# Kernel optimization log

Hardware: AMD Instinct MI355X
Metric: run time of the kernel (lower is better)

Reference implementation:

```python
import jax, jax.numpy as jnp
import numpy as np

DIM = 1024
NUM_HEADS = 16
HEAD_DIM = DIM // NUM_HEADS
SCALE = HEAD_DIM ** -0.5


def setup_inputs() -> dict:
    key = jax.random.key(0)
    ks = jax.random.split(key, 9)
    s = 1.0 / np.sqrt(DIM)
    x = jax.random.normal(ks[0], (2, 2048, DIM), dtype=jnp.float32)
    Wq = jax.random.normal(ks[1], (DIM, DIM), dtype=jnp.float32) * s
    Wk = jax.random.normal(ks[2], (DIM, DIM), dtype=jnp.float32) * s
    Wv = jax.random.normal(ks[3], (DIM, DIM), dtype=jnp.float32) * s
    Wp = jax.random.normal(ks[4], (DIM, DIM), dtype=jnp.float32) * s
    bq = jax.random.normal(ks[5], (DIM,), dtype=jnp.float32) * s
    bk = jax.random.normal(ks[6], (DIM,), dtype=jnp.float32) * s
    bv = jax.random.normal(ks[7], (DIM,), dtype=jnp.float32) * s
    bp = jax.random.normal(ks[8], (DIM,), dtype=jnp.float32) * s
    return {"x": x, "Wq": Wq, "bq": bq, "Wk": Wk, "bk": bk,
            "Wv": Wv, "bv": bv, "Wp": Wp, "bp": bp}


def reference(x, Wq, bq, Wk, bk, Wv, bv, Wp, bp):
    B, L, C = x.shape
    H, D = NUM_HEADS, HEAD_DIM
    # Linear projections (torch Linear: x @ W.T + b)
    q = x @ Wq.T + bq
    k = x @ Wk.T + bk
    v = x @ Wv.T + bv
    # (B, L, H*D) -> (B, H, L, D)
    q = q.reshape(B, L, H, D).transpose(0, 2, 1, 3)
    k = k.reshape(B, L, H, D).transpose(0, 2, 1, 3)
    v = v.reshape(B, L, H, D).transpose(0, 2, 1, 3)
    # scaled dot-product attention, full L x L scores (as in source)
    attn = jnp.einsum('bhqd,bhkd->bhqk', q, k) * SCALE
    attn = jax.nn.softmax(attn, axis=-1)
    out = jnp.einsum('bhqk,bhkd->bhqd', attn, v)
    out = out.transpose(0, 2, 1, 3).reshape(B, L, C)
    return out @ Wp.T + bp
```

## Files before the change

kernel.cpp:

```cpp
#include <hip/hip_runtime.h>

#define DIMC 1024
#define SEQL 2048
#define NB   2
#define NH   16
#define HD   64
#define MTOT (NB*SEQL)
#define XSTR 2048
static constexpr float SM_SCALE = 0.125f;
static constexpr float LOG2E    = 1.4426950408889634f;
static constexpr float QSCALE   = SM_SCALE * LOG2E;

typedef short s16x8 __attribute__((ext_vector_type(8)));
typedef short s16x4 __attribute__((ext_vector_type(4)));
typedef float f32x4 __attribute__((ext_vector_type(4)));
typedef int   i32x4 __attribute__((ext_vector_type(4)));

__device__ __forceinline__ unsigned short f2bf(float f) {
    unsigned int u = __float_as_uint(f);
    u += 0x7fffu + ((u >> 16) & 1u);
    return (unsigned short)(u >> 16);
}
__device__ __forceinline__ s16x8 ld8(const unsigned short* p) {
    return *(const s16x8*)p;
}
__device__ __forceinline__ void gld_lds16(const unsigned short* g, unsigned short* l) {
    __builtin_amdgcn_global_load_lds(
        (const __attribute__((address_space(1))) void*)g,
        (__attribute__((address_space(3))) void*)l, 16, 0, 0);
}

__global__ __launch_bounds__(256) void cast_all(
    const float* __restrict__ x,
    const float* __restrict__ Wq, const float* __restrict__ Wk,
    const float* __restrict__ Wv, const float* __restrict__ Wp,
    const float* __restrict__ bq, const float* __restrict__ bk,
    const float* __restrict__ bvv,
    unsigned short* __restrict__ xb, unsigned short* __restrict__ wall,
    float* __restrict__ ball)
{
    const int bid = blockIdx.x, tid = threadIdx.x;
    if (bid < 4096) {
        int i = bid * 256 + tid;
        float4 f = ((const float4*)x)[i];
        s16x4 o;
        o[0] = (short)f2bf(f.x); o[1] = (short)f2bf(f.y);
        o[2] = (short)f2bf(f.z); o[3] = (short)f2bf(f.w);
        ((s16x4*)xb)[i] = o;
    } else if (bid < 8192) {
        int j = (bid - 4096) * 256 + tid;
        int r = j >> 18;
        const float* src = (r == 0) ? Wq : (r == 1) ? Wk : (r == 2) ? Wv : Wp;
        float4 f = ((const float4*)src)[j & 262143];
        s16x4 o;
        o[0] = (short)f2bf(f.x); o[1] = (short)f2bf(f.y);
        o[2] = (short)f2bf(f.z); o[3] = (short)f2bf(f.w);
        ((s16x4*)wall)[j] = o;
    } else {
        int t2 = (bid - 8192) * 256 + tid;
        if (t2 < 3072)
            ball[t2] = (t2 < 1024) ? bq[t2]
                     : (t2 < 2048) ? bk[t2 - 1024] : bvv[t2 - 2048];
    }
}

__global__ __launch_bounds__(256) void gemm_tile(
    const unsigned short* __restrict__ A, int astride,
    const unsigned short* __restrict__ Wb,
    const float* __restrict__ bias,
    unsigned short* qk, unsigned short* vtb, float* outf, int mode)
{
    __shared__ __align__(16) unsigned short Asm[128 * 32];
    __shared__ __align__(16) unsigned short Bsm[128 * 32];

    const int t    = threadIdx.x;
    const int lane = t & 63;
    const int l15  = lane & 15;
    const int quad = lane >> 4;
    const int w    = t >> 6;
    const int mrow = (w & 1) * 64;
    const int ncol = (w >> 1) * 64;
    const int mt   = blockIdx.x & 31;
    const int nt   = blockIdx.x >> 5;
    const int row0 = mt * 128;

    const unsigned short* ga = A  + (size_t)(row0 + (t >> 2)) * astride + (t & 3) * 8;
    const unsigned short* gb = Wb + (size_t)(nt * 128 + (t >> 2)) * DIMC + (t & 3) * 8;
    const size_t gaStep = (size_t)64 * astride;
    const size_t gbStep = (size_t)64 * DIMC;

    f32x4 acc[4][4] = {};

    for (int k0 = 0; k0 < DIMC; k0 += 32) {
        gld_lds16(ga + k0,          Asm + t * 8);
        gld_lds16(ga + gaStep + k0, Asm + 2048 + t * 8);
        gld_lds16(gb + k0,          Bsm + t * 8);
        gld_lds16(gb + gbStep + k0, Bsm + 2048 + t * 8);
        __syncthreads();

        s16x8 a[4], b[4];
#pragma unroll
        for (int mi = 0; mi < 4; ++mi)
            a[mi] = *(const s16x8*)(Asm + (mrow + mi * 16 + l15) * 32 + quad * 8);
#pragma unroll
        for (int ni = 0; ni < 4; ++ni)
            b[ni] = *(const s16x8*)(Bsm + (ncol + ni * 16 + l15) * 32 + quad * 8);
#pragma unroll
        for (int mi = 0; mi < 4; ++mi)
#pragma unroll
            for (int ni = 0; ni < 4; ++ni)
                acc[mi][ni] = __builtin_amdgcn_mfma_f32_16x16x32_bf16(
                    a[mi], b[ni], acc[mi][ni], 0, 0, 0);
        __syncthreads();
    }

    const int proj = nt >> 3;
#pragma unroll
    for (int ni = 0; ni < 4; ++ni) {
        const int cq = (nt & 7) * 128 + ncol + ni * 16 + l15;
        const float bz = bias[proj * 1024 + cq];
#pragma unroll
        for (int mi = 0; mi < 4; ++mi) {
            const int rbase = row0 + mrow + mi * 16 + quad * 4;
            if (mode == 0) {
                if (proj < 2) {
                    const float scale = (proj == 0) ? QSCALE : 1.0f;
#pragma unroll
                    for (int r = 0; r < 4; ++r)
                        qk[(size_t)(rbase + r) * XSTR + proj * DIMC + cq] =
                            f2bf((acc[mi][ni][r] + bz) * scale);
                } else {
                    const int h = cq >> 6, d = cq & 63;
                    const int bb = rbase >> 11, ll = rbase & (SEQL - 1);
                    s16x4 v4;
                    v4[0] = (short)f2bf(acc[mi][ni][0] + bz);
                    v4[1] = (short)f2bf(acc[mi][ni][1] + bz);
                    v4[2] = (short)f2bf(acc[mi][ni][2] + bz);
                    v4[3] = (short)f2bf(acc[mi][ni][3] + bz);
                    *(s16x4*)(vtb + ((size_t)((bb * NH + h) * HD + d)) * SEQL + ll) = v4;
                }
            } else {
#pragma unroll
                for (int r = 0; r < 4; ++r)
                    outf[(size_t)(rbase + r) * DIMC + cq] = acc[mi][ni][r] + bz;
            }
        }
    }
}

__global__ __launch_bounds__(128) void attn_fused(
    unsigned short* xqk,
    const unsigned short* __restrict__ vt)
{
    __shared__ __align__(16) unsigned short Ksm[2][64 * 64];
    __shared__ __align__(16) unsigned short Vsm[2][64 * 64];

    const int t    = threadIdx.x;
    const int lane = t & 63;
    const int l15  = lane & 15;
    const int quad = lane >> 4;
    const int w    = t >> 6;

    const int bh = blockIdx.x >> 5;
    const int qb = blockIdx.x & 31;
    const int h  = bh & (NH - 1);
    const int bb = bh >> 4;
    const int q0A = qb * 64 + w * 16;
    const int q0B = q0A + 32;

    unsigned short* qbase = xqk + (size_t)(bb * SEQL) * XSTR + h * HD + quad * 8;
    unsigned short* qrA = qbase + (size_t)(q0A + l15) * XSTR;
    unsigned short* qrB = qbase + (size_t)(q0B + l15) * XSTR;
    const s16x8 bqA0 = ld8(qrA), bqA1 = ld8(qrA + 32);
    const s16x8 bqB0 = ld8(qrB), bqB1 = ld8(qrB + 32);

    const int tr = t >> 3, tp = t & 7;
    const int swz = (tp ^ (tr & 7)) * 8;
    const unsigned short* kg = xqk + (size_t)bb * SEQL * XSTR + DIMC + h * HD
                               + (size_t)tr * XSTR + swz;
    const unsigned short* vg = vt + (size_t)(bh * HD + tr) * SEQL + swz;

    f32x4 oA[4] = {}, oB[4] = {};
    float lsA = 0.f, lsB = 0.f;
    const int xk = l15 & 7;

#pragma unroll
    for (int g = 0; g < 4; ++g) {
        gld_lds16(kg + (size_t)(g * 16) * XSTR, Ksm[0] + g * 1024 + t * 8);
        gld_lds16(vg + (size_t)(g * 16) * SEQL, Vsm[0] + g * 1024 + t * 8);
    }
    __syncthreads();

    for (int j0 = 0; j0 < SEQL; j0 += 64) {
        const int cur = (j0 >> 6) & 1, nxt = cur ^ 1;
        if (j0 + 64 < SEQL) {
            const int jn = j0 + 64;
#pragma unroll
            for (int g = 0; g < 4; ++g) {
                gld_lds16(kg + (size_t)(jn + g * 16) * XSTR, Ksm[nxt] + g * 1024 + t * 8);
                gld_lds16(vg + (size_t)(g * 16) * SEQL + jn,  Vsm[nxt] + g * 1024 + t * 8);
            }
        }
        const unsigned short* Kc = Ksm[cur];
        const unsigned short* Vc = Vsm[cur];

#pragma unroll
        for (int hf = 0; hf < 2; ++hf) {
            const int k0 = (hf * 32 + l15) * 64;
            const int k1 = (hf * 32 + 16 + l15) * 64;
            s16x8 a00 = *(const s16x8*)(Kc + k0 + ((quad       ^ xk) * 8));
            s16x8 a01 = *(const s16x8*)(Kc + k0 + (((quad + 4) ^ xk) * 8));
            s16x8 a10 = *(const s16x8*)(Kc + k1 + ((quad       ^ xk) * 8));
            s16x8 a11 = *(const s16x8*)(Kc + k1 + (((quad + 4) ^ xk) * 8));

            s16x8 bv[4];
#pragma unroll
            for (int c = 0; c < 4; ++c) {
                const unsigned short* va = Vc + (c * 16 + l15) * 64 + (quad & 1) * 4;
                const int kc0 = hf * 4 + (quad >> 1);
                s16x4 v0 = *(const s16x4*)(va + ((kc0       ^ xk) * 8));
                s16x4 v1 = *(const s16x4*)(va + (((kc0 + 2) ^ xk) * 8));
                bv[c] = __builtin_shufflevector(v0, v1, 0, 1, 2, 3, 4, 5, 6, 7);
            }

            {
                f32x4 st0 = {}, st1 = {};
                st0 = __builtin_amdgcn_mfma_f32_16x16x32_bf16(a00, bqA0, st0, 0, 0, 0);
                st0 = __builtin_amdgcn_mfma_f32_16x16x32_bf16(a01, bqA1, st0, 0, 0, 0);
                st1 = __builtin_amdgcn_mfma_f32_16x16x32_bf16(a10, bqA0, st1, 0, 0, 0);
                st1 = __builtin_amdgcn_mfma_f32_16x16x32_bf16(a11, bqA1, st1, 0, 0, 0);
                unsigned int t0[4], t1[4];
#pragma unroll
                for (int r = 0; r < 4; ++r) {
                    t0[r] = __float_as_uint(__builtin_amdgcn_exp2f(st0[r])) & 0xffff0000u;
                    t1[r] = __float_as_uint(__builtin_amdgcn_exp2f(st1[r])) & 0xffff0000u;
                    lsA += __uint_as_float(t0[r]) + __uint_as_float(t1[r]);
                }
                i32x4 api;
                api[0] = (int)((t0[0] >> 16) | t0[1]);
                api[1] = (int)((t0[2] >> 16) | t0[3]);
                api[2] = (int)((t1[0] >> 16) | t1[1]);
                api[3] = (int)((t1[2] >> 16) | t1[3]);
                s16x8 ap = __builtin_bit_cast(s16x8, api);
#pragma unroll
                for (int c = 0; c < 4; ++c)
                    oA[c] = __builtin_amdgcn_mfma_f32_16x16x32_bf16(ap, bv[c], oA[c], 0, 0, 0);
            }
            {
                f32x4 st0 = {}, st1 = {};
                st0 = __builtin_amdgcn_mfma_f32_16x16x32_bf16(a00, bqB0, st0, 0, 0, 0);
                st0 = __builtin_amdgcn_mfma_f32_16x16x32_bf16(a01, bqB1, st0, 0, 0, 0);
                st1 = __builtin_amdgcn_mfma_f32_16x16x32_bf16(a10, bqB0, st1, 0, 0, 0);
                st1 = __builtin_amdgcn_mfma_f32_16x16x32_bf16(a11, bqB1, st1, 0, 0, 0);
                unsigned int t0[4], t1[4];
#pragma unroll
                for (int r = 0; r < 4; ++r) {
                    t0[r] = __float_as_uint(__builtin_amdgcn_exp2f(st0[r])) & 0xffff0000u;
                    t1[r] = __float_as_uint(__builtin_amdgcn_exp2f(st1[r])) & 0xffff0000u;
                    lsB += __uint_as_float(t0[r]) + __uint_as_float(t1[r]);
                }
                i32x4 api;
                api[0] = (int)((t0[0] >> 16) | t0[1]);
                api[1] = (int)((t0[2] >> 16) | t0[3]);
                api[2] = (int)((t1[0] >> 16) | t1[1]);
                api[3] = (int)((t1[2] >> 16) | t1[3]);
                s16x8 ap = __builtin_bit_cast(s16x8, api);
#pragma unroll
                for (int c = 0; c < 4; ++c)
                    oB[c] = __builtin_amdgcn_mfma_f32_16x16x32_bf16(ap, bv[c], oB[c], 0, 0, 0);
            }
        }
        __syncthreads();
    }

    lsA += __shfl_xor(lsA, 16);  lsA += __shfl_xor(lsA, 32);
    lsB += __shfl_xor(lsB, 16);  lsB += __shfl_xor(lsB, 32);

    float liA[4], liB[4];
#pragma unroll
    for (int r = 0; r < 4; ++r) {
        liA[r] = 1.0f / __shfl(lsA, quad * 4 + r, 64);
        liB[r] = 1.0f / __shfl(lsB, quad * 4 + r, 64);
    }

#pragma unroll
    for (int c = 0; c < 4; ++c) {
        const int d = c * 16 + l15;
#pragma unroll
        for (int r = 0; r < 4; ++r) {
            const int qr = quad * 4 + r;
            xqk[(size_t)(bb * SEQL + q0A + qr) * XSTR + h * HD + d] = f2bf(oA[c][r] * liA[r]);
            xqk[(size_t)(bb * SEQL + q0B + qr) * XSTR + h * HD + d] = f2bf(oB[c][r] * liB[r]);
        }
    }
}

extern "C" void kernel_launch(void* const* d_in, const int* in_sizes, int n_in,
                              void* d_out, int out_size, void* d_ws, size_t ws_size,
                              hipStream_t stream) {
    const float* x  = (const float*)d_in[0];
    const float* Wq = (const float*)d_in[1];
    const float* bq = (const float*)d_in[2];
    const float* Wk = (const float*)d_in[3];
    const float* bk = (const float*)d_in[4];
    const float* Wv = (const float*)d_in[5];
    const float* bv = (const float*)d_in[6];
    const float* Wp = (const float*)d_in[7];
    const float* bp = (const float*)d_in[8];
    float* out = (float*)d_out;
    unsigned short* vtb = (unsigned short*)d_out;
    unsigned short* xqk = (unsigned short*)d_in[0];

    unsigned short* ws   = (unsigned short*)d_ws;
    const size_t XELT = (size_t)MTOT * DIMC;
    const size_t WELT = (size_t)DIMC * DIMC;
    unsigned short* xb   = ws;
    unsigned short* wall = ws + XELT;
    float*          ball = (float*)(ws + 2 * XELT);

    cast_all<<<8204, 256, 0, stream>>>(x, Wq, Wk, Wv, Wp, bq, bk, bv, xb, wall, ball);

    gemm_tile<<<768, 256, 0, stream>>>(xb, DIMC, wall, ball, xqk, vtb, nullptr, 0);

    attn_fused<<<NB * NH * (SEQL / 64), 128, 0, stream>>>(xqk, vtb);

    gemm_tile<<<256, 256, 0, stream>>>(xqk, XSTR, wall + 3 * WELT, bp,
                                       nullptr, nullptr, out, 1);
}
```

Before: 229.4 us.

## Compute softmax row sums via MFMA with ones, packed bf16 convert, XCD-aware block mapping

The softmax denominator is now accumulated by an extra MFMA against a vector of bf16 ones instead of scalar VALU adds, which also removes the final cross-lane shuffles. The exp results are packed with v_cvt_pk_bf16_f32 (round-to-nearest) instead of truncation masks and shifts. Blocks are remapped so consecutive block IDs on the same XCD share a batch-head, aiming at better L2 reuse of K/V. The change trades VALU work for one extra MFMA per tile and slightly alters rounding.

```diff
diff --git a/kernel.cpp b/kernel.cpp
--- a/kernel.cpp
+++ b/kernel.cpp
@@ -28,6 +28,11 @@
     __builtin_amdgcn_global_load_lds(
         (const __attribute__((address_space(1))) void*)g,
         (__attribute__((address_space(3))) void*)l, 16, 0, 0);
+}
+__device__ __forceinline__ unsigned int cvtpk(float lo, float hi) {
+    unsigned int r;
+    asm("v_cvt_pk_bf16_f32 %0, %1, %2" : "=v"(r) : "v"(lo), "v"(hi));
+    return r;
 }
 
 __global__ __launch_bounds__(256) void cast_all(
@@ -161,8 +166,10 @@
     const int quad = lane >> 4;
     const int w    = t >> 6;
 
-    const int bh = blockIdx.x >> 5;
-    const int qb = blockIdx.x & 31;
+    const int xcd = blockIdx.x & 7;
+    const int ii  = blockIdx.x >> 3;
+    const int bh  = (xcd << 2) | (ii >> 5);
+    const int qb  = ii & 31;
     const int h  = bh & (NH - 1);
     const int bb = bh >> 4;
     const int q0A = qb * 64 + w * 16;
@@ -174,6 +181,10 @@
     const s16x8 bqA0 = ld8(qrA), bqA1 = ld8(qrA + 32);
     const s16x8 bqB0 = ld8(qrB), bqB1 = ld8(qrB + 32);
 
+    s16x8 bones;
+#pragma unroll
+    for (int e = 0; e < 8; ++e) bones[e] = (short)0x3F80;
+
     const int tr = t >> 3, tp = t & 7;
     const int swz = (tp ^ (tr & 7)) * 8;
     const unsigned short* kg = xqk + (size_t)bb * SEQL * XSTR + DIMC + h * HD
@@ -181,7 +192,7 @@
     const unsigned short* vg = vt + (size_t)(bh * HD + tr) * SEQL + swz;
 
     f32x4 oA[4] = {}, oB[4] = {};
-    float lsA = 0.f, lsB = 0.f;
+    f32x4 laccA = {}, laccB = {};
     const int xk = l15 & 7;
 
 #pragma unroll
@@ -229,19 +240,17 @@
                 st0 = __builtin_amdgcn_mfma_f32_16x16x32_bf16(a01, bqA1, st0, 0, 0, 0);
                 st1 = __builtin_amdgcn_mfma_f32_16x16x32_bf16(a10, bqA0, st1, 0, 0, 0);
                 st1 = __builtin_amdgcn_mfma_f32_16x16x32_bf16(a11, bqA1, st1, 0, 0, 0);
-                unsigned int t0[4], t1[4];
-#pragma unroll
-                for (int r = 0; r < 4; ++r) {
-                    t0[r] = __float_as_uint(__builtin_amdgcn_exp2f(st0[r])) & 0xffff0000u;
-                    t1[r] = __float_as_uint(__builtin_amdgcn_exp2f(st1[r])) & 0xffff0000u;
-                    lsA += __uint_as_float(t0[r]) + __uint_as_float(t1[r]);
-                }
                 i32x4 api;
-                api[0] = (int)((t0[0] >> 16) | t0[1]);
-                api[1] = (int)((t0[2] >> 16) | t0[3]);
-                api[2] = (int)((t1[0] >> 16) | t1[1]);
-                api[3] = (int)((t1[2] >> 16) | t1[3]);
+                api[0] = (int)cvtpk(__builtin_amdgcn_exp2f(st0[0]),
+                                    __builtin_amdgcn_exp2f(st0[1]));
+                api[1] = (int)cvtpk(__builtin_amdgcn_exp2f(st0[2]),
+                                    __builtin_amdgcn_exp2f(st0[3]));
+                api[2] = (int)cvtpk(__builtin_amdgcn_exp2f(st1[0]),
+                                    __builtin_amdgcn_exp2f(st1[1]));
+                api[3] = (int)cvtpk(__builtin_amdgcn_exp2f(st1[2]),
+                                    __builtin_amdgcn_exp2f(st1[3]));
                 s16x8 ap = __builtin_bit_cast(s16x8, api);
+                laccA = __builtin_amdgcn_mfma_f32_16x16x32_bf16(ap, bones, laccA, 0, 0, 0);
 #pragma unroll
                 for (int c = 0; c < 4; ++c)
                     oA[c] = __builtin_amdgcn_mfma_f32_16x16x32_bf16(ap, bv[c], oA[c], 0, 0, 0);
@@ -252,19 +261,17 @@
                 st0 = __builtin_amdgcn_mfma_f32_16x16x32_bf16(a01, bqB1, st0, 0, 0, 0);
                 st1 = __builtin_amdgcn_mfma_f32_16x16x32_bf16(a10, bqB0, st1, 0, 0, 0);
                 st1 = __builtin_amdgcn_mfma_f32_16x16x32_bf16(a11, bqB1, st1, 0, 0, 0);
-                unsigned int t0[4], t1[4];
-#pragma unroll
-                for (int r = 0; r < 4; ++r) {
-                    t0[r] = __float_as_uint(__builtin_amdgcn_exp2f(st0[r])) & 0xffff0000u;
-                    t1[r] = __float_as_uint(__builtin_amdgcn_exp2f(st1[r])) & 0xffff0000u;
-                    lsB += __uint_as_float(t0[r]) + __uint_as_float(t1[r]);
-                }
                 i32x4 api;
-                api[0] = (int)((t0[0] >> 16) | t0[1]);
-                api[1] = (int)((t0[2] >> 16) | t0[3]);
-                api[2] = (int)((t1[0] >> 16) | t1[1]);
-                api[3] = (int)((t1[2] >> 16) | t1[3]);
+                api[0] = (int)cvtpk(__builtin_amdgcn_exp2f(st0[0]),
+                                    __builtin_amdgcn_exp2f(st0[1]));
+                api[1] = (int)cvtpk(__builtin_amdgcn_exp2f(st0[2]),
+                                    __builtin_amdgcn_exp2f(st0[3]));
+                api[2] = (int)cvtpk(__builtin_amdgcn_exp2f(st1[0]),
+                                    __builtin_amdgcn_exp2f(st1[1]));
+                api[3] = (int)cvtpk(__builtin_amdgcn_exp2f(st1[2]),
+                                    __builtin_amdgcn_exp2f(st1[3]));
                 s16x8 ap = __builtin_bit_cast(s16x8, api);
+                laccB = __builtin_amdgcn_mfma_f32_16x16x32_bf16(ap, bones, laccB, 0, 0, 0);
 #pragma unroll
                 for (int c = 0; c < 4; ++c)
                     oB[c] = __builtin_amdgcn_mfma_f32_16x16x32_bf16(ap, bv[c], oB[c], 0, 0, 0);
@@ -273,14 +280,11 @@
         __syncthreads();
     }
 
-    lsA += __shfl_xor(lsA, 16);  lsA += __shfl_xor(lsA, 32);
-    lsB += __shfl_xor(lsB, 16);  lsB += __shfl_xor(lsB, 32);
-
     float liA[4], liB[4];
 #pragma unroll
     for (int r = 0; r < 4; ++r) {
-        liA[r] = 1.0f / __shfl(lsA, quad * 4 + r, 64);
-        liB[r] = 1.0f / __shfl(lsB, quad * 4 + r, 64);
+        liA[r] = 1.0f / laccA[r];
+        liB[r] = 1.0f / laccB[r];
     }
 
 #pragma unroll
```

Result: faster. 220.7 us (-3.8%).
